# Optimization experiments

Measured on AMD Instinct MI355X. Metric: run time of the kernel, lower is better.

The kernel has to match this reference:

```python
import jax, jax.numpy as jnp
import numpy as np

B, C, IC, H, W = 4, 256, 128, 64, 64
EPS = 1e-5  # BatchNorm eps (eval mode, running stats)


def conv_bn(x, w, b, gamma, beta, mean, var, relu):
    # 1x1 conv == channel contraction; BN in eval mode (affine w/ running stats)
    y = jnp.einsum('oc,bchw->bohw', w, x) + b[None, :, None, None]
    scale = gamma * jax.lax.rsqrt(var + EPS)
    shift = beta - mean * scale
    y = y * scale[None, :, None, None] + shift[None, :, None, None]
    return jax.nn.relu(y) if relu else y


def setup_inputs() -> dict:
    key = jax.random.key(0)
    ks = jax.random.split(key, 32)

    def branch(i, co, ci):
        return dict(
            w=jax.random.normal(ks[i], (co, ci), jnp.float32) * 0.05,
            b=jax.random.normal(ks[i + 1], (co,), jnp.float32) * 0.05,
            gamma=jax.random.uniform(ks[i + 2], (co,), jnp.float32, 0.5, 1.5),
            beta=jax.random.normal(ks[i + 3], (co,), jnp.float32) * 0.05,
            mean=jax.random.normal(ks[i + 4], (co,), jnp.float32) * 0.05,
            var=jax.random.uniform(ks[i + 5], (co,), jnp.float32, 0.5, 1.5),
        )

    g = branch(0, IC, C)
    th = branch(6, IC, C)
    ph = branch(12, IC, C)
    wo = branch(18, C, IC)
    inp = {'x': jax.random.normal(ks[24], (B, C, H, W), jnp.float32)}
    for pre, p in (('g', g), ('th', th), ('ph', ph), ('w', wo)):
        for k, v in p.items():
            inp[f'{pre}_{k}'] = v
    return inp


def reference(x, g_w, g_b, g_gamma, g_beta, g_mean, g_var,
              th_w, th_b, th_gamma, th_beta, th_mean, th_var,
              ph_w, ph_b, ph_gamma, ph_beta, ph_mean, ph_var,
              w_w, w_b, w_gamma, w_beta, w_mean, w_var):
    b, c, h, w = x.shape
    ic = g_w.shape[0]
    g_x = conv_bn(x, g_w, g_b, g_gamma, g_beta, g_mean, g_var, True).reshape(b, ic, h * w)     # [b,ic,n]
    theta = conv_bn(x, th_w, th_b, th_gamma, th_beta, th_mean, th_var, True).reshape(b, ic, h * w)
    phi = conv_bn(x, ph_w, ph_b, ph_gamma, ph_beta, ph_mean, ph_var, True).reshape(b, ic, h * w)
    # unscaled attention over flattened spatial positions
    f = jnp.einsum('bcn,bcm->bnm', theta, phi)     # [b,n,n]
    a = jax.nn.softmax(f, axis=2)
    y = jnp.einsum('bnm,bcm->bcn', a, g_x)         # [b,ic,n]
    y = y.reshape(b, ic, h, w)
    y = conv_bn(y, w_w, w_b, w_gamma, w_beta, w_mean, w_var, False)
    return y + x
```

## Files before the change

kernel.cpp:

```cpp
#include <hip/hip_runtime.h>
#include <math.h>

typedef __attribute__((ext_vector_type(8))) short short8;
typedef __attribute__((ext_vector_type(8))) _Float16 half8;
typedef __attribute__((ext_vector_type(4))) float f32x4;

#define NSP 4096
#define CIN 256
#define ICH 128
#define SPLITS 4
#define TILES_PER_SPLIT 16

__device__ __forceinline__ unsigned short f2h(float x){
  union { _Float16 h; unsigned short u; } v; v.h = (_Float16)x; return v.u;
}
__device__ __forceinline__ float h2f(unsigned short u){
  union { _Float16 h; unsigned short u; } v; v.u = u; return (float)v.h;
}
__device__ __forceinline__ unsigned pk2h(float a, float b){
  union { __fp16 __attribute__((ext_vector_type(2))) v; unsigned u; } r;
  r.v = __builtin_amdgcn_cvt_pkrtz(a, b);
  return r.u;
}
__device__ __forceinline__ int swz(int row, int e){ return e ^ ((row & 7) << 3); }

__device__ __forceinline__ f32x4 mfmah(short8 a, short8 b, f32x4 c){
  union { short8 s; half8 h; } ua, ub; ua.s = a; ub.s = b;
  return __builtin_amdgcn_mfma_f32_16x16x32_f16(ua.h, ub.h, c, 0, 0, 0);
}

__device__ __forceinline__ void st4h(unsigned short* p, unsigned short a, unsigned short b,
                                     unsigned short c, unsigned short d){
  ushort4 v; v.x=a; v.y=b; v.z=c; v.w=d;
  *(ushort4*)p = v;
}

__device__ __forceinline__ void gload_lds16(const unsigned short* g, unsigned short* l){
  __builtin_amdgcn_global_load_lds(
      (const __attribute__((address_space(1))) unsigned int*)g,
      (__attribute__((address_space(3))) unsigned int*)l, 16, 0, 0);
}

__device__ __forceinline__ void stage_nc(const unsigned short* gbase, unsigned short* lds,
                                         int w, int l){
  #pragma unroll
  for (int i=0;i<4;++i){
    int rl = 16*w + 4*i + (l>>4);
    int eg = ((l&15)*8) ^ ((rl&7)<<3);
    gload_lds16(gbase + (size_t)rl*128 + eg, lds + w*2048 + i*512);
  }
}
__device__ __forceinline__ void stage_cn(const unsigned short* gbase, unsigned short* lds,
                                         int w, int l){
  #pragma unroll
  for (int i=0;i<4;++i){
    int cl = 32*w + 8*i + (l>>3);
    int me = ((l&7)*8) ^ ((cl&7)<<3);
    gload_lds16(gbase + (size_t)cl*NSP + me, lds + w*2048 + i*512);
  }
}

__global__ __launch_bounds__(256) void conv_fused_k(
    const float* __restrict__ x,
    const float* __restrict__ w0, const float* __restrict__ b0,
    const float* __restrict__ ga0, const float* __restrict__ be0,
    const float* __restrict__ me0, const float* __restrict__ va0,
    const float* __restrict__ w1, const float* __restrict__ b1,
    const float* __restrict__ ga1, const float* __restrict__ be1,
    const float* __restrict__ me1, const float* __restrict__ va1,
    const float* __restrict__ w2, const float* __restrict__ b2,
    const float* __restrict__ ga2, const float* __restrict__ be2,
    const float* __restrict__ me2, const float* __restrict__ va2,
    unsigned short* __restrict__ outg, unsigned short* __restrict__ outt,
    unsigned short* __restrict__ outp)
{
  const int b = blockIdx.z, nt = blockIdx.x, ot = blockIdx.y;
  const int n0 = nt*64, o0 = ot*64;
  const int t = threadIdx.x, w = t>>6, l = t&63;
  __shared__ unsigned short xs[64][64];
  __shared__ unsigned short ws[3][64][64];
  __shared__ float sc_s[3][64], sh_s[3][64];
  if (t < 64){
    int o = o0 + t;
    float s0 = ga0[o]*rsqrtf(va0[o]+1e-5f);
    sc_s[0][t]=s0; sh_s[0][t]=be0[o]-me0[o]*s0+b0[o]*s0;
    float s1 = ga1[o]*rsqrtf(va1[o]+1e-5f);
    sc_s[1][t]=s1; sh_s[1][t]=be1[o]-me1[o]*s1+b1[o]*s1;
    float s2 = ga2[o]*rsqrtf(va2[o]+1e-5f);
    sc_s[2][t]=s2; sh_s[2][t]=be2[o]-me2[o]*s2+b2[o]*s2;
  }
  const f32x4 Z = {0.f,0.f,0.f,0.f};
  f32x4 acc[3][4];
  #pragma unroll
  for (int br=0;br<3;++br) for (int i=0;i<4;++i) acc[br][i] = Z;
  const float* Wt[3] = {w0, w1, w2};

  for (int kc = 0; kc < CIN; kc += 64){
    __syncthreads();
    #pragma unroll
    for (int p = 0; p < 4; ++p){
      int cw = p*16 + (t>>4);
      int q4 = (t&15)*4;
      float4 xv = *(const float4*)(x + ((size_t)b*CIN + kc + cw)*NSP + n0 + q4);
      float xa[4] = {xv.x, xv.y, xv.z, xv.w};
      #pragma unroll
      for (int i=0;i<4;++i){
        int r = q4 + i;
        xs[r][swz(r, cw)] = f2h(xa[i]);
      }
      #pragma unroll
      for (int br=0;br<3;++br){
        float4 wv = *(const float4*)(Wt[br] + (size_t)(o0 + cw)*CIN + kc + q4);
        int cs = swz(cw, q4);
        st4h(&ws[br][cw][cs], f2h(wv.x), f2h(wv.y), f2h(wv.z), f2h(wv.w));
      }
    }
    __syncthreads();
    #pragma unroll
    for (int kf = 0; kf < 2; ++kf){
      int ko = kf*32 + (l>>4)*8;
      int wr = 16*w + (l&15);
      short8 wf0 = *(const short8*)&ws[0][wr][swz(wr, ko)];
      short8 wf1 = *(const short8*)&ws[1][wr][swz(wr, ko)];
      short8 wf2 = *(const short8*)&ws[2][wr][swz(wr, ko)];
      #pragma unroll
      for (int nf = 0; nf < 4; ++nf){
        int xr = 16*nf + (l&15);
        short8 xf = *(const short8*)&xs[xr][swz(xr, ko)];
        acc[0][nf] = mfmah(wf0, xf, acc[0][nf]);
        acc[1][nf] = mfmah(xf, wf1, acc[1][nf]);
        acc[2][nf] = mfmah(xf, wf2, acc[2][nf]);
      }
    }
  }
  #pragma unroll
  for (int j=0;j<4;++j){
    int ol = 16*w + (l>>4)*4 + j;
    float s = sc_s[0][ol], sh = sh_s[0][ol];
    #pragma unroll
    for (int nf=0;nf<4;++nf){
      int n = n0 + 16*nf + (l&15);
      float v = fmaxf(acc[0][nf][j]*s + sh, 0.f);
      outg[((size_t)b*ICH + o0 + ol)*NSP + n] = f2h(v);
    }
  }
  {
    int ol = 16*w + (l&15);
    float s1 = sc_s[1][ol], sh1 = sh_s[1][ol];
    float s2 = sc_s[2][ol], sh2 = sh_s[2][ol];
    #pragma unroll
    for (int nf=0; nf<4; ++nf)
      #pragma unroll
      for (int j=0;j<4;++j){
        int n = n0 + 16*nf + (l>>4)*4 + j;
        float v1 = fmaxf(acc[1][nf][j]*s1 + sh1, 0.f);
        float v2 = fmaxf(acc[2][nf][j]*s2 + sh2, 0.f);
        outt[((size_t)b*NSP + n)*ICH + o0 + ol] = f2h(v1);
        outp[((size_t)b*NSP + n)*ICH + o0 + ol] = f2h(v2);
      }
  }
}

__global__ __launch_bounds__(256, 2) void attn_k(
  const unsigned short* __restrict__ thp, const unsigned short* __restrict__ php,
  const unsigned short* __restrict__ gb, unsigned short* __restrict__ ypart,
  float* __restrict__ ml)
{
  const int bx = blockIdx.x;
  const int xcd = bx & 7, jj = bx >> 3;
  const int combo = xcd*2 + (jj>>5);
  const int qt = jj & 31;
  const int b = combo & 3, s = combo >> 2;
  const int n0 = qt*128;
  const int t = threadIdx.x, w = t>>6, l = t&63;

  __shared__ unsigned short kb[2][64][128];
  __shared__ unsigned short vb[2][128][64];
  __shared__ unsigned short ps[128][64];

  stage_nc(thp + ((size_t)b*NSP + n0      )*ICH, &kb[0][0][0], w, l);
  stage_nc(thp + ((size_t)b*NSP + n0 + 64 )*ICH, &kb[1][0][0], w, l);
  __syncthreads();
  short8 qf0[4], qf1[4];
  {
    int qr = 16*w + (l&15);
    #pragma unroll
    for (int kf=0;kf<4;++kf){
      int ko = kf*32 + (l>>4)*8;
      qf0[kf] = *(const short8*)&kb[0][qr][swz(qr, ko)];
      qf1[kf] = *(const short8*)&kb[1][qr][swz(qr, ko)];
    }
  }
  __syncthreads();

  const f32x4 Z = {0.f,0.f,0.f,0.f};
  f32x4 oa0[8], oa1[8];
  #pragma unroll
  for (int i=0;i<8;++i){ oa0[i]=Z; oa1[i]=Z; }
  float m0r = -1e30f, m1r = -1e30f;
  float l0r = 0.f, l1r = 0.f;

  const int tile0 = s*TILES_PER_SPLIT;
  stage_nc(php + ((size_t)b*NSP + tile0*64)*ICH, &kb[0][0][0], w, l);
  stage_cn(gb + (size_t)b*ICH*NSP + tile0*64,    &vb[0][0][0], w, l);
  __syncthreads();
  int cur = 0;

  for (int it = 0; it < TILES_PER_SPLIT; ++it){
    if (it < TILES_PER_SPLIT-1){
      int m0n = (tile0 + it + 1)*64;
      stage_nc(php + ((size_t)b*NSP + m0n)*ICH, &kb[cur^1][0][0], w, l);
      stage_cn(gb + (size_t)b*ICH*NSP + m0n,    &vb[cur^1][0][0], w, l);
    }
    f32x4 f0[4], f1[4];
    #pragma unroll
    for (int i=0;i<4;++i){ f0[i]=Z; f1[i]=Z; }
    __builtin_amdgcn_s_setprio(1);
    #pragma unroll
    for (int mf=0; mf<4; ++mf){
      int kr = 16*mf + (l&15);
      #pragma unroll
      for (int kf=0; kf<4; ++kf){
        short8 bh = *(const short8*)&kb[cur][kr][swz(kr, kf*32 + (l>>4)*8)];
        f0[mf] = mfmah(bh, qf0[kf], f0[mf]);
        f1[mf] = mfmah(bh, qf1[kf], f1[mf]);
      }
    }
    __builtin_amdgcn_s_setprio(0);

    #pragma unroll
    for (int h=0; h<2; ++h){
      f32x4* f = h ? f1 : f0;
      float& mr = h ? m1r : m0r;
      float& lr = h ? l1r : l0r;
      f32x4* oa = h ? oa1 : oa0;
      float mx = f[0][0];
      #pragma unroll
      for (int mf=0;mf<4;++mf)
        #pragma unroll
        for (int j=0;j<4;++j) mx = fmaxf(mx, f[mf][j]);
      mx = fmaxf(mx, __shfl_xor(mx, 16));
      mx = fmaxf(mx, __shfl_xor(mx, 32));
      if (__any(mx - mr > 8.f)){
        float mn = fmaxf(mr, mx);
        float al = __expf(mr - mn);
        mr = mn; lr *= al;
        #pragma unroll
        for (int j=0;j<4;++j){
          float alj = __shfl(al, (l>>4)*4 + j);
          #pragma unroll
          for (int cf=0;cf<8;++cf) oa[cf][j] *= alj;
        }
      }
      float sm = 0.f;
      #pragma unroll
      for (int mf=0;mf<4;++mf)
        #pragma unroll
        for (int j=0;j<4;++j){
          float pv = __expf(f[mf][j] - mr);
          f[mf][j] = pv;
          sm += pv;
        }
      sm += __shfl_xor(sm, 16);
      sm += __shfl_xor(sm, 32);
      lr += sm;
      int r = h*64 + 16*w + (l&15);
      int cb = 4*(l>>4);
      #pragma unroll
      for (int mf=0;mf<4;++mf)
        #pragma unroll
        for (int p=0;p<2;++p){
          unsigned pk = pk2h(f[mf][2*p], f[mf][2*p+1]);
          int cc = 16*mf + cb + 2*p;
          *(unsigned*)&ps[r][swz(r,cc)] = pk;
        }
    }

    __builtin_amdgcn_s_setprio(1);
    {
      int pr0 = 16*w + (l&15), pr1 = 64 + pr0;
      #pragma unroll
      for (int mk=0;mk<2;++mk){
        int ko = mk*32 + (l>>4)*8;
        short8 ap0 = *(const short8*)&ps[pr0][swz(pr0,ko)];
        short8 ap1 = *(const short8*)&ps[pr1][swz(pr1,ko)];
        #pragma unroll
        for (int cf=0;cf<8;++cf){
          int vr = 16*cf + (l&15);
          short8 bv = *(const short8*)&vb[cur][vr][swz(vr,ko)];
          oa0[cf] = mfmah(ap0, bv, oa0[cf]);
          oa1[cf] = mfmah(ap1, bv, oa1[cf]);
        }
      }
    }
    __builtin_amdgcn_s_setprio(0);

    __syncthreads();
    cur ^= 1;
  }

  #pragma unroll
  for (int h=0; h<2; ++h){
    float mr = h ? m1r : m0r;
    float lr = h ? l1r : l0r;
    f32x4* oa = h ? oa1 : oa0;
    float invl = 1.f / lr;
    #pragma unroll
    for (int j=0;j<4;++j){
      float inv = __shfl(invl, (l>>4)*4 + j);
      int n = n0 + h*64 + 16*w + (l>>4)*4 + j;
      #pragma unroll
      for (int cf=0;cf<8;++cf){
        int c = 16*cf + (l&15);
        ypart[(((size_t)s*4 + b)*NSP + n)*ICH + c] = f2h(oa[cf][j]*inv);
      }
    }
    if (l < 16){
      int n = n0 + h*64 + 16*w + l;
      ml[(((size_t)s*4 + b)*NSP + n)*2 + 0] = mr;
      ml[(((size_t)s*4 + b)*NSP + n)*2 + 1] = lr;
    }
  }
}

__global__ __launch_bounds__(256) void final_k(
  const unsigned short* __restrict__ ypart, const float* __restrict__ ml,
  const float* __restrict__ x, const float* __restrict__ Wm,
  const float* __restrict__ bias, const float* __restrict__ gamma,
  const float* __restrict__ beta, const float* __restrict__ mean,
  const float* __restrict__ var, float* __restrict__ out)
{
  const int b = blockIdx.z, ot = blockIdx.y, nt = blockIdx.x;
  const int n0 = nt*64, o0 = ot*64;
  const int t = threadIdx.x, w = t>>6, l = t&63;
  __shared__ unsigned short ys[64][128];
  __shared__ unsigned short w2s[64][128];
  __shared__ float wc[SPLITS][64];
  __shared__ float sc_s[64], sh_s[64];
  if (t < 64){
    int o = o0 + t;
    float s = gamma[o]*rsqrtf(var[o]+1e-5f);
    sc_s[t]=s; sh_s[t]=beta[o]-mean[o]*s+bias[o]*s;
  } else if (t < 128){
    int r = t - 64, n = n0 + r;
    float mv[SPLITS], lv[SPLITS];
    #pragma unroll
    for (int s=0;s<SPLITS;++s){
      mv[s] = ml[(((size_t)s*4 + b)*NSP + n)*2 + 0];
      lv[s] = ml[(((size_t)s*4 + b)*NSP + n)*2 + 1];
    }
    float M = fmaxf(fmaxf(mv[0],mv[1]), fmaxf(mv[2],mv[3]));
    float wsum = 0.f, wv[SPLITS];
    #pragma unroll
    for (int s=0;s<SPLITS;++s){ wv[s] = lv[s]*__expf(mv[s]-M); wsum += wv[s]; }
    float inv = 1.f/wsum;
    #pragma unroll
    for (int s=0;s<SPLITS;++s) wc[s][r] = wv[s]*inv;
  }
  __syncthreads();
  #pragma unroll
  for (int p=0;p<4;++p){
    int id = p*256 + t, r = id>>4, c8 = (id&15)*8;
    float accv[8] = {0,0,0,0,0,0,0,0};
    #pragma unroll
    for (int s=0;s<SPLITS;++s){
      short8 v = *(const short8*)(ypart + (((size_t)s*4 + b)*NSP + n0 + r)*ICH + c8);
      float wgt = wc[s][r];
      #pragma unroll
      for (int i=0;i<8;++i) accv[i] += wgt * h2f(((unsigned short*)&v)[i]);
    }
    unsigned short hv[8];
    #pragma unroll
    for (int i=0;i<8;++i) hv[i] = f2h(accv[i]);
    *(short8*)&ys[r][swz(r,c8)] = *(short8*)hv;

    float4 u0 = *(const float4*)(Wm + (size_t)(o0 + r)*ICH + c8);
    float4 u1 = *(const float4*)(Wm + (size_t)(o0 + r)*ICH + c8 + 4);
    unsigned short wh[8] = {f2h(u0.x),f2h(u0.y),f2h(u0.z),f2h(u0.w),
                            f2h(u1.x),f2h(u1.y),f2h(u1.z),f2h(u1.w)};
    *(short8*)&w2s[r][swz(r,c8)] = *(short8*)wh;
  }
  __syncthreads();
  const f32x4 Z = {0.f,0.f,0.f,0.f};
  f32x4 acc[4];
  for (int i=0;i<4;++i) acc[i]=Z;
  #pragma unroll
  for (int kf=0;kf<4;++kf){
    int ko = kf*32 + (l>>4)*8;
    int wr = 16*w + (l&15);
    short8 a = *(const short8*)&w2s[wr][swz(wr,ko)];
    #pragma unroll
    for (int nf=0;nf<4;++nf){
      int yr = 16*nf + (l&15);
      short8 bb = *(const short8*)&ys[yr][swz(yr,ko)];
      acc[nf] = mfmah(a, bb, acc[nf]);
    }
  }
  #pragma unroll
  for (int j=0;j<4;++j){
    int ol = 16*w + (l>>4)*4 + j;
    float s = sc_s[ol], sh = sh_s[ol];
    #pragma unroll
    for (int nf=0;nf<4;++nf){
      int n = n0 + 16*nf + (l&15);
      size_t idx = ((size_t)b*CIN + o0 + ol)*NSP + n;
      out[idx] = acc[nf][j]*s + sh + x[idx];
    }
  }
}

extern "C" void kernel_launch(void* const* d_in, const int* in_sizes, int n_in,
                              void* d_out, int out_size, void* d_ws, size_t ws_size,
                              hipStream_t stream){
  const float* x    = (const float*)d_in[0];
  const float* g_w  = (const float*)d_in[1];
  const float* g_b  = (const float*)d_in[2];
  const float* g_ga = (const float*)d_in[3];
  const float* g_be = (const float*)d_in[4];
  const float* g_me = (const float*)d_in[5];
  const float* g_va = (const float*)d_in[6];
  const float* t_w  = (const float*)d_in[7];
  const float* t_b  = (const float*)d_in[8];
  const float* t_ga = (const float*)d_in[9];
  const float* t_be = (const float*)d_in[10];
  const float* t_me = (const float*)d_in[11];
  const float* t_va = (const float*)d_in[12];
  const float* p_w  = (const float*)d_in[13];
  const float* p_b  = (const float*)d_in[14];
  const float* p_ga = (const float*)d_in[15];
  const float* p_be = (const float*)d_in[16];
  const float* p_me = (const float*)d_in[17];
  const float* p_va = (const float*)d_in[18];
  const float* w_w  = (const float*)d_in[19];
  const float* w_b  = (const float*)d_in[20];
  const float* w_ga = (const float*)d_in[21];
  const float* w_be = (const float*)d_in[22];
  const float* w_me = (const float*)d_in[23];
  const float* w_va = (const float*)d_in[24];

  char* ws = (char*)d_ws;
  const size_t SEG = (size_t)4*NSP*ICH*sizeof(unsigned short);
  unsigned short* th_t  = (unsigned short*)(ws);
  unsigned short* ph_t  = (unsigned short*)(ws + SEG);
  unsigned short* g_cn  = (unsigned short*)(ws + 2*SEG);
  unsigned short* ypart = (unsigned short*)(ws + 3*SEG);
  float*          mlb   = (float*)(ws + 3*SEG + SPLITS*SEG);

  dim3 blk(256,1,1);
  conv_fused_k<<<dim3(64,2,4), blk, 0, stream>>>(
      x,
      g_w, g_b, g_ga, g_be, g_me, g_va,
      t_w, t_b, t_ga, t_be, t_me, t_va,
      p_w, p_b, p_ga, p_be, p_me, p_va,
      g_cn, th_t, ph_t);
  attn_k<<<dim3(512,1,1), blk, 0, stream>>>(th_t, ph_t, g_cn, ypart, mlb);
  final_k<<<dim3(64,4,4), blk, 0, stream>>>(ypart, mlb, x, w_w, w_b, w_ga, w_be, w_me, w_va, (float*)d_out);
}
```

Measured before the change: 74.71 us.

## Keep softmax probabilities in registers and fold log2e into theta projection

The attention kernel no longer writes P to shared memory. It packs the probabilities into registers and uses them directly as the MFMA A operand, which requires permuting the g output layout along the key dimension to match the register fragment order. The log2(e) factor is folded into the theta BN scale so the softmax can use exp2, and the rescale threshold is widened to match. The V buffer is reduced to a single buffer loaded each iteration, with explicit waitcnt and barriers, and Q is loaded through that buffer. This cuts LDS footprint and traffic, but removes double-buffering of V, which may expose load latency.

```diff
diff --git a/kernel.cpp b/kernel.cpp
--- a/kernel.cpp
+++ b/kernel.cpp
@@ -10,6 +10,7 @@
 #define ICH 128
 #define SPLITS 4
 #define TILES_PER_SPLIT 16
+#define LOG2E 1.44269504088896f
 
 __device__ __forceinline__ unsigned short f2h(float x){
   union { _Float16 h; unsigned short u; } v; v.h = (_Float16)x; return v.u;
@@ -58,6 +59,10 @@
     int me = ((l&7)*8) ^ ((cl&7)<<3);
     gload_lds16(gbase + (size_t)cl*NSP + me, lds + w*2048 + i*512);
   }
+}
+
+__device__ __forceinline__ int kperm(int q){
+  return ((q>>4)&1)*4 + ((q>>2)&3)*8 + (q&3);
 }
 
 __global__ __launch_bounds__(256) void conv_fused_k(
@@ -85,7 +90,7 @@
     float s0 = ga0[o]*rsqrtf(va0[o]+1e-5f);
     sc_s[0][t]=s0; sh_s[0][t]=be0[o]-me0[o]*s0+b0[o]*s0;
     float s1 = ga1[o]*rsqrtf(va1[o]+1e-5f);
-    sc_s[1][t]=s1; sh_s[1][t]=be1[o]-me1[o]*s1+b1[o]*s1;
+    sc_s[1][t]=s1*LOG2E; sh_s[1][t]=(be1[o]-me1[o]*s1+b1[o]*s1)*LOG2E;
     float s2 = ga2[o]*rsqrtf(va2[o]+1e-5f);
     sc_s[2][t]=s2; sh_s[2][t]=be2[o]-me2[o]*s2+b2[o]*s2;
   }
@@ -140,8 +145,9 @@
     #pragma unroll
     for (int nf=0;nf<4;++nf){
       int n = n0 + 16*nf + (l&15);
+      int nst = (n & ~31) | kperm(n & 31);
       float v = fmaxf(acc[0][nf][j]*s + sh, 0.f);
-      outg[((size_t)b*ICH + o0 + ol)*NSP + n] = f2h(v);
+      outg[((size_t)b*ICH + o0 + ol)*NSP + nst] = f2h(v);
     }
   }
   {
@@ -175,23 +181,29 @@
   const int t = threadIdx.x, w = t>>6, l = t&63;
 
   __shared__ unsigned short kb[2][64][128];
-  __shared__ unsigned short vb[2][128][64];
-  __shared__ unsigned short ps[128][64];
-
-  stage_nc(thp + ((size_t)b*NSP + n0      )*ICH, &kb[0][0][0], w, l);
-  stage_nc(thp + ((size_t)b*NSP + n0 + 64 )*ICH, &kb[1][0][0], w, l);
-  __syncthreads();
+  __shared__ unsigned short vbuf[128][64];
+  unsigned short* vbf = &vbuf[0][0];
+
   short8 qf0[4], qf1[4];
   {
     int qr = 16*w + (l&15);
-    #pragma unroll
-    for (int kf=0;kf<4;++kf){
-      int ko = kf*32 + (l>>4)*8;
-      qf0[kf] = *(const short8*)&kb[0][qr][swz(qr, ko)];
-      qf1[kf] = *(const short8*)&kb[1][qr][swz(qr, ko)];
-    }
-  }
-  __syncthreads();
+    stage_nc(thp + ((size_t)b*NSP + n0)*ICH, vbf, w, l);
+    asm volatile("s_waitcnt vmcnt(0)" ::: "memory");
+    __builtin_amdgcn_s_barrier();
+    __builtin_amdgcn_sched_barrier(0);
+    #pragma unroll
+    for (int kf=0;kf<4;++kf)
+      qf0[kf] = *(const short8*)&vbf[qr*128 + swz(qr, kf*32 + (l>>4)*8)];
+    __builtin_amdgcn_s_barrier();
+    stage_nc(thp + ((size_t)b*NSP + n0 + 64)*ICH, vbf, w, l);
+    asm volatile("s_waitcnt vmcnt(0)" ::: "memory");
+    __builtin_amdgcn_s_barrier();
+    __builtin_amdgcn_sched_barrier(0);
+    #pragma unroll
+    for (int kf=0;kf<4;++kf)
+      qf1[kf] = *(const short8*)&vbf[qr*128 + swz(qr, kf*32 + (l>>4)*8)];
+    __builtin_amdgcn_s_barrier();
+  }
 
   const f32x4 Z = {0.f,0.f,0.f,0.f};
   f32x4 oa0[8], oa1[8];
@@ -199,19 +211,20 @@
   for (int i=0;i<8;++i){ oa0[i]=Z; oa1[i]=Z; }
   float m0r = -1e30f, m1r = -1e30f;
   float l0r = 0.f, l1r = 0.f;
+  unsigned pk0[8], pk1[8];
 
   const int tile0 = s*TILES_PER_SPLIT;
   stage_nc(php + ((size_t)b*NSP + tile0*64)*ICH, &kb[0][0][0], w, l);
-  stage_cn(gb + (size_t)b*ICH*NSP + tile0*64,    &vb[0][0][0], w, l);
-  __syncthreads();
+  asm volatile("s_waitcnt vmcnt(0)" ::: "memory");
+  __builtin_amdgcn_s_barrier();
+  __builtin_amdgcn_sched_barrier(0);
   int cur = 0;
 
   for (int it = 0; it < TILES_PER_SPLIT; ++it){
-    if (it < TILES_PER_SPLIT-1){
-      int m0n = (tile0 + it + 1)*64;
-      stage_nc(php + ((size_t)b*NSP + m0n)*ICH, &kb[cur^1][0][0], w, l);
-      stage_cn(gb + (size_t)b*ICH*NSP + m0n,    &vb[cur^1][0][0], w, l);
-    }
+    stage_cn(gb + (size_t)b*ICH*NSP + (tile0+it)*64, vbf, w, l);
+    if (it < TILES_PER_SPLIT-1)
+      stage_nc(php + ((size_t)b*NSP + (tile0+it+1)*64)*ICH, &kb[cur^1][0][0], w, l);
+
     f32x4 f0[4], f1[4];
     #pragma unroll
     for (int i=0;i<4;++i){ f0[i]=Z; f1[i]=Z; }
@@ -234,6 +247,7 @@
       float& mr = h ? m1r : m0r;
       float& lr = h ? l1r : l0r;
       f32x4* oa = h ? oa1 : oa0;
+      unsigned* pk = h ? pk1 : pk0;
       float mx = f[0][0];
       #pragma unroll
       for (int mf=0;mf<4;++mf)
@@ -241,9 +255,9 @@
         for (int j=0;j<4;++j) mx = fmaxf(mx, f[mf][j]);
       mx = fmaxf(mx, __shfl_xor(mx, 16));
       mx = fmaxf(mx, __shfl_xor(mx, 32));
-      if (__any(mx - mr > 8.f)){
+      if (__any(mx - mr > 11.5f)){
         float mn = fmaxf(mr, mx);
-        float al = __expf(mr - mn);
+        float al = exp2f(mr - mn);
         mr = mn; lr *= al;
         #pragma unroll
         for (int j=0;j<4;++j){
@@ -257,45 +271,49 @@
       for (int mf=0;mf<4;++mf)
         #pragma unroll
         for (int j=0;j<4;++j){
-          float pv = __expf(f[mf][j] - mr);
+          float pv = exp2f(f[mf][j] - mr);
           f[mf][j] = pv;
           sm += pv;
         }
       sm += __shfl_xor(sm, 16);
       sm += __shfl_xor(sm, 32);
       lr += sm;
-      int r = h*64 + 16*w + (l&15);
-      int cb = 4*(l>>4);
       #pragma unroll
       for (int mf=0;mf<4;++mf)
         #pragma unroll
-        for (int p=0;p<2;++p){
-          unsigned pk = pk2h(f[mf][2*p], f[mf][2*p+1]);
-          int cc = 16*mf + cb + 2*p;
-          *(unsigned*)&ps[r][swz(r,cc)] = pk;
-        }
-    }
+        for (int p=0;p<2;++p)
+          pk[2*mf+p] = pk2h(f[mf][2*p], f[mf][2*p+1]);
+    }
+
+    if (it < TILES_PER_SPLIT-1)
+      asm volatile("s_waitcnt vmcnt(4)" ::: "memory");
+    else
+      asm volatile("s_waitcnt vmcnt(0)" ::: "memory");
+    __builtin_amdgcn_s_barrier();
+    __builtin_amdgcn_sched_barrier(0);
 
     __builtin_amdgcn_s_setprio(1);
     {
-      int pr0 = 16*w + (l&15), pr1 = 64 + pr0;
+      int g8 = (l>>4)*8;
       #pragma unroll
       for (int mk=0;mk<2;++mk){
-        int ko = mk*32 + (l>>4)*8;
-        short8 ap0 = *(const short8*)&ps[pr0][swz(pr0,ko)];
-        short8 ap1 = *(const short8*)&ps[pr1][swz(pr1,ko)];
+        union { unsigned u[4]; short8 s8; } a0u, a1u;
+        #pragma unroll
+        for (int q=0;q<4;++q){ a0u.u[q] = pk0[4*mk+q]; a1u.u[q] = pk1[4*mk+q]; }
         #pragma unroll
         for (int cf=0;cf<8;++cf){
           int vr = 16*cf + (l&15);
-          short8 bv = *(const short8*)&vb[cur][vr][swz(vr,ko)];
-          oa0[cf] = mfmah(ap0, bv, oa0[cf]);
-          oa1[cf] = mfmah(ap1, bv, oa1[cf]);
+          short8 bv = *(const short8*)&vbf[vr*64 + swz(vr, mk*32 + g8)];
+          oa0[cf] = mfmah(a0u.s8, bv, oa0[cf]);
+          oa1[cf] = mfmah(a1u.s8, bv, oa1[cf]);
         }
       }
     }
     __builtin_amdgcn_s_setprio(0);
 
-    __syncthreads();
+    asm volatile("s_waitcnt vmcnt(0)" ::: "memory");
+    __builtin_amdgcn_s_barrier();
+    __builtin_amdgcn_sched_barrier(0);
     cur ^= 1;
   }
 
@@ -352,7 +370,7 @@
     float M = fmaxf(fmaxf(mv[0],mv[1]), fmaxf(mv[2],mv[3]));
     float wsum = 0.f, wv[SPLITS];
     #pragma unroll
-    for (int s=0;s<SPLITS;++s){ wv[s] = lv[s]*__expf(mv[s]-M); wsum += wv[s]; }
+    for (int s=0;s<SPLITS;++s){ wv[s] = lv[s]*exp2f(mv[s]-M); wsum += wv[s]; }
     float inv = 1.f/wsum;
     #pragma unroll
     for (int s=0;s<SPLITS;++s) wc[s][r] = wv[s]*inv;
```

New measurement: 80.06 us. 7.2% more time.

## Keep softmax probabilities in registers via permuted V layout and exp2 domain

Applied to the files above, without the earlier changes.

The g projection output is stored with a permuted spatial order inside each 32-element group, so the P fragments produced by the QK MFMA can be fed straight into the PV MFMA as A operands. This removes the LDS round trip through the ps buffer. Separately, the log2(e) factor is folded into the theta BN scale so the softmax uses exp2f directly, and the rescale threshold is adjusted to match the base-2 domain. The cost is a coupled layout contract between the conv and attention kernels; any later reader of g must use the same permutation.

```diff
diff --git a/kernel.cpp b/kernel.cpp
--- a/kernel.cpp
+++ b/kernel.cpp
@@ -10,6 +10,7 @@
 #define ICH 128
 #define SPLITS 4
 #define TILES_PER_SPLIT 16
+#define LOG2E 1.44269504088896f
 
 __device__ __forceinline__ unsigned short f2h(float x){
   union { _Float16 h; unsigned short u; } v; v.h = (_Float16)x; return v.u;
@@ -58,6 +59,10 @@
     int me = ((l&7)*8) ^ ((cl&7)<<3);
     gload_lds16(gbase + (size_t)cl*NSP + me, lds + w*2048 + i*512);
   }
+}
+
+__device__ __forceinline__ int kperm(int q){
+  return ((q>>4)&1)*4 + ((q>>2)&3)*8 + (q&3);
 }
 
 __global__ __launch_bounds__(256) void conv_fused_k(
@@ -85,7 +90,7 @@
     float s0 = ga0[o]*rsqrtf(va0[o]+1e-5f);
     sc_s[0][t]=s0; sh_s[0][t]=be0[o]-me0[o]*s0+b0[o]*s0;
     float s1 = ga1[o]*rsqrtf(va1[o]+1e-5f);
-    sc_s[1][t]=s1; sh_s[1][t]=be1[o]-me1[o]*s1+b1[o]*s1;
+    sc_s[1][t]=s1*LOG2E; sh_s[1][t]=(be1[o]-me1[o]*s1+b1[o]*s1)*LOG2E;
     float s2 = ga2[o]*rsqrtf(va2[o]+1e-5f);
     sc_s[2][t]=s2; sh_s[2][t]=be2[o]-me2[o]*s2+b2[o]*s2;
   }
@@ -140,8 +145,9 @@
     #pragma unroll
     for (int nf=0;nf<4;++nf){
       int n = n0 + 16*nf + (l&15);
+      int nst = (n & ~31) | kperm(n & 31);
       float v = fmaxf(acc[0][nf][j]*s + sh, 0.f);
-      outg[((size_t)b*ICH + o0 + ol)*NSP + n] = f2h(v);
+      outg[((size_t)b*ICH + o0 + ol)*NSP + nst] = f2h(v);
     }
   }
   {
@@ -176,7 +182,6 @@
 
   __shared__ unsigned short kb[2][64][128];
   __shared__ unsigned short vb[2][128][64];
-  __shared__ unsigned short ps[128][64];
 
   stage_nc(thp + ((size_t)b*NSP + n0      )*ICH, &kb[0][0][0], w, l);
   stage_nc(thp + ((size_t)b*NSP + n0 + 64 )*ICH, &kb[1][0][0], w, l);
@@ -199,6 +204,7 @@
   for (int i=0;i<8;++i){ oa0[i]=Z; oa1[i]=Z; }
   float m0r = -1e30f, m1r = -1e30f;
   float l0r = 0.f, l1r = 0.f;
+  unsigned pk0[8], pk1[8];
 
   const int tile0 = s*TILES_PER_SPLIT;
   stage_nc(php + ((size_t)b*NSP + tile0*64)*ICH, &kb[0][0][0], w, l);
@@ -212,6 +218,7 @@
       stage_nc(php + ((size_t)b*NSP + m0n)*ICH, &kb[cur^1][0][0], w, l);
       stage_cn(gb + (size_t)b*ICH*NSP + m0n,    &vb[cur^1][0][0], w, l);
     }
+
     f32x4 f0[4], f1[4];
     #pragma unroll
     for (int i=0;i<4;++i){ f0[i]=Z; f1[i]=Z; }
@@ -234,6 +241,7 @@
       float& mr = h ? m1r : m0r;
       float& lr = h ? l1r : l0r;
       f32x4* oa = h ? oa1 : oa0;
+      unsigned* pk = h ? pk1 : pk0;
       float mx = f[0][0];
       #pragma unroll
       for (int mf=0;mf<4;++mf)
@@ -241,9 +249,9 @@
         for (int j=0;j<4;++j) mx = fmaxf(mx, f[mf][j]);
       mx = fmaxf(mx, __shfl_xor(mx, 16));
       mx = fmaxf(mx, __shfl_xor(mx, 32));
-      if (__any(mx - mr > 8.f)){
+      if (__any(mx - mr > 11.5f)){
         float mn = fmaxf(mr, mx);
-        float al = __expf(mr - mn);
+        float al = exp2f(mr - mn);
         mr = mn; lr *= al;
         #pragma unroll
         for (int j=0;j<4;++j){
@@ -257,39 +265,34 @@
       for (int mf=0;mf<4;++mf)
         #pragma unroll
         for (int j=0;j<4;++j){
-          float pv = __expf(f[mf][j] - mr);
+          float pv = exp2f(f[mf][j] - mr);
           f[mf][j] = pv;
           sm += pv;
         }
       sm += __shfl_xor(sm, 16);
       sm += __shfl_xor(sm, 32);
       lr += sm;
-      int r = h*64 + 16*w + (l&15);
-      int cb = 4*(l>>4);
       #pragma unroll
       for (int mf=0;mf<4;++mf)
         #pragma unroll
-        for (int p=0;p<2;++p){
-          unsigned pk = pk2h(f[mf][2*p], f[mf][2*p+1]);
-          int cc = 16*mf + cb + 2*p;
-          *(unsigned*)&ps[r][swz(r,cc)] = pk;
-        }
+        for (int p=0;p<2;++p)
+          pk[2*mf+p] = pk2h(f[mf][2*p], f[mf][2*p+1]);
     }
 
     __builtin_amdgcn_s_setprio(1);
     {
-      int pr0 = 16*w + (l&15), pr1 = 64 + pr0;
+      int g8 = (l>>4)*8;
       #pragma unroll
       for (int mk=0;mk<2;++mk){
-        int ko = mk*32 + (l>>4)*8;
-        short8 ap0 = *(const short8*)&ps[pr0][swz(pr0,ko)];
-        short8 ap1 = *(const short8*)&ps[pr1][swz(pr1,ko)];
+        union { unsigned u[4]; short8 s8; } a0u, a1u;
+        #pragma unroll
+        for (int q=0;q<4;++q){ a0u.u[q] = pk0[4*mk+q]; a1u.u[q] = pk1[4*mk+q]; }
         #pragma unroll
         for (int cf=0;cf<8;++cf){
           int vr = 16*cf + (l&15);
-          short8 bv = *(const short8*)&vb[cur][vr][swz(vr,ko)];
-          oa0[cf] = mfmah(ap0, bv, oa0[cf]);
-          oa1[cf] = mfmah(ap1, bv, oa1[cf]);
+          short8 bv = *(const short8*)&vb[cur][vr][swz(vr, mk*32 + g8)];
+          oa0[cf] = mfmah(a0u.s8, bv, oa0[cf]);
+          oa1[cf] = mfmah(a1u.s8, bv, oa1[cf]);
         }
       }
     }
@@ -352,7 +355,7 @@
     float M = fmaxf(fmaxf(mv[0],mv[1]), fmaxf(mv[2],mv[3]));
     float wsum = 0.f, wv[SPLITS];
     #pragma unroll
-    for (int s=0;s<SPLITS;++s){ wv[s] = lv[s]*__expf(mv[s]-M); wsum += wv[s]; }
+    for (int s=0;s<SPLITS;++s){ wv[s] = lv[s]*exp2f(mv[s]-M); wsum += wv[s]; }
     float inv = 1.f/wsum;
     #pragma unroll
     for (int s=0;s<SPLITS;++s) wc[s][r] = wv[s]*inv;
```

After: 80.27 us. 1.07x slower.
